# Performance work log

Measured on AMD Instinct MI355X. Metric: run time of the kernel, lower is better.

## Reference

```python
import jax, jax.numpy as jnp
import numpy as np

N = 50000      # nodes
E = 800000     # edges (avg degree 16)
F_IN = 128
# (d_in, d_out) for the 9 GCNConv layers with width=256, n_layers=3
DIMS = [(128, 128), (128, 192), (192, 256), (256, 256), (256, 256), (256, 256), (256, 192), (192, 128), (128, 1)]
# ReLU after every conv except loop conv i==n_layers-2 (conv idx 4) and the final conv
RELU = [True, True, True, True, False, True, True, True, False]


def setup_inputs() -> dict:
    key = jax.random.key(0)
    ks = jax.random.split(key, 2 + 2 * len(DIMS))
    inp = {
        "x": jax.random.normal(ks[0], (N, F_IN), dtype=jnp.float32),
        "edge_index": jax.random.randint(ks[1], (2, E), 0, N, dtype=jnp.int64),
    }
    for i, (din, dout) in enumerate(DIMS):
        # Glorot-ish init for weights, small random bias (GCNConv has bias=True)
        inp[f"W{i}"] = jax.random.normal(ks[2 + 2 * i], (din, dout), dtype=jnp.float32) / np.float32(np.sqrt(din))
        inp[f"b{i}"] = jax.random.normal(ks[3 + 2 * i], (dout,), dtype=jnp.float32) * 0.01
    return inp


def _gcn_stack(x, src_f, dst_f, norm, Ws, bs):
    h = x
    for i in range(len(Ws)):
        h = h @ Ws[i]                                  # [N, dout] dense transform first (dout <= din mostly)
        msg = h[src_f] * norm[:, None]                 # gather + edge-normalize  [E+N, dout]
        h = jax.ops.segment_sum(msg, dst_f, num_segments=N) + bs[i]
        if RELU[i]:
            h = jax.nn.relu(h)
        # Dropout layers are identity in eval/inference mode.
    return h


def reference(x, edge_index,
              W0, b0, W1, b1, W2, b2, W3, b3, W4, b4, W5, b5, W6, b6, W7, b7, W8, b8):
    src, dst = edge_index[0], edge_index[1]
    loop = jnp.arange(N, dtype=src.dtype)
    # GCNConv default: add self loops, symmetric normalization D^{-1/2}(A+I)D^{-1/2}
    src_f = jnp.concatenate([src, loop])
    dst_f = jnp.concatenate([dst, loop])
    deg = jax.ops.segment_sum(jnp.ones(E + N, dtype=x.dtype), dst_f, num_segments=N)
    dinv = jax.lax.rsqrt(jnp.maximum(deg, 1.0))        # deg >= 1 thanks to self loops
    norm = dinv[src_f] * dinv[dst_f]                   # per-edge coefficient [E+N]
    Ws = [W0, W1, W2, W3, W4, W5, W6, W7, W8]
    bs = [b0, b1, b2, b3, b4, b5, b6, b7, b8]
    return _gcn_stack(x, src_f, dst_f, norm, Ws, bs)   # [N, 1]
```

## Files before the change

kernel.cpp:

```cpp
#include <hip/hip_runtime.h>


#define TPB 256

using bf16x8 = __attribute__((ext_vector_type(8))) __bf16;
using f32x4  = __attribute__((ext_vector_type(4))) float;
using f32x2  = __attribute__((ext_vector_type(2))) float;

__device__ __forceinline__ unsigned bf16rne(float x) {
    unsigned u = __float_as_uint(x);
    return (u + 0x7fffu + ((u >> 16) & 1u)) >> 16;
}

__device__ __forceinline__ f32x2 bl2(unsigned u) {
    return (f32x2){__uint_as_float(u << 16), __uint_as_float(u & 0xffff0000u)};
}

__device__ __forceinline__ void stage16(const unsigned short* g, unsigned short* l) {
#if __has_builtin(__builtin_amdgcn_global_load_lds)
    __builtin_amdgcn_global_load_lds((const __attribute__((address_space(1))) void*)g,
                                     (__attribute__((address_space(3))) void*)l, 16, 0, 0);
#else
    *(uint4*)((char*)l + (threadIdx.x & 63) * 16) = *(const uint4*)g;
#endif
}


__global__ void zinit_kernel(int* cnt, int n) {
    int i = blockIdx.x * blockDim.x + threadIdx.x;
    if (i < n) cnt[i] = 0;
}

__global__ void count_kernel(const int* __restrict__ dst, int* __restrict__ cnt,
                             int* __restrict__ rank, int E) {
    int e = blockIdx.x * blockDim.x + threadIdx.x;
    if (e < E) rank[e] = atomicAdd(&cnt[dst[e]], 1);
}


__global__ void blockhist_kernel(const int* __restrict__ cnt, int* __restrict__ localRank,
                                 int* __restrict__ hb, float* __restrict__ dinv,
                                 int n, int nb) {
    __shared__ int h[64];
    int t = threadIdx.x;
    if (t < 64) h[t] = 0;
    __syncthreads();
    int i = blockIdx.x * TPB + t;
    if (i < n) {
        int c = cnt[i];
        dinv[i] = rsqrtf((float)(c + 1));
        int d = c; if (d > 63) d = 63;
        localRank[i] = atomicAdd(&h[d], 1);
    }
    __syncthreads();
    if (t < 64) hb[t * nb + blockIdx.x] = h[t];
}

__global__ __launch_bounds__(256) void sortscan_kernel(int* __restrict__ hb, int nb) {
    __shared__ int sh[64 * 256];
    __shared__ int tot[64], base[64];
    int t = threadIdx.x;
    int total = 64 * nb;
    for (int i = t; i < total; i += 256) sh[i] = hb[i];
    __syncthreads();
    if (t < 64) {
        int run = 0;
        for (int b = 0; b < nb; b++) {
            int v = sh[t * nb + b];
            sh[t * nb + b] = run;
            run += v;
        }
        tot[t] = run;
    }
    __syncthreads();
    if (t == 0) {
        int acc = 0;
        for (int b = 0; b < 64; b++) { base[b] = acc; acc += tot[b]; }
    }
    __syncthreads();
    for (int i = t; i < total; i += 256) hb[i] = sh[i] + base[i / nb];
}

__global__ void scatter2_kernel(const int* __restrict__ cnt,
                                const int* __restrict__ localRank, const int* __restrict__ hb,
                                int* __restrict__ perm, int* __restrict__ pcnt,
                                int* __restrict__ iperm, int n, int nb) {
    int i = blockIdx.x * TPB + threadIdx.x;
    if (i >= n) return;
    int c = cnt[i];
    int d = c; if (d > 63) d = 63;
    int pos = hb[d * nb + blockIdx.x] + localRank[i];
    perm[pos] = i;
    pcnt[pos] = c;
    iperm[i] = pos;
}

__global__ void scan1_kernel(const int* __restrict__ pcnt, int* __restrict__ prowp2,
                             int* __restrict__ bsums, int n) {
    __shared__ int sh[TPB];
    int t = threadIdx.x;
    int i = blockIdx.x * TPB + t;
    int v = (i < n) ? (pcnt[i] + 1) : 0;
    sh[t] = v;
    __syncthreads();
    for (int off = 1; off < TPB; off <<= 1) {
        int x = (t >= off) ? sh[t - off] : 0;
        __syncthreads();
        sh[t] += x;
        __syncthreads();
    }
    if (i < n) prowp2[i] = sh[t] - v;
    if (t == TPB - 1) bsums[blockIdx.x] = sh[t];
}

__global__ void scan3_kernel(int* __restrict__ rowp, const int* __restrict__ bsums,
                             int n, int nb) {
    __shared__ int sh[TPB];
    int t = threadIdx.x;
    int v = (t < nb && t < (int)blockIdx.x) ? bsums[t] : 0;
    sh[t] = v;
    __syncthreads();
    for (int off = 1; off < TPB; off <<= 1) {
        int x = (t >= off) ? sh[t - off] : 0;
        __syncthreads();
        sh[t] += x;
        __syncthreads();
    }
    int offset = sh[TPB - 1];
    int i = blockIdx.x * TPB + t;
    if (i < n) rowp[i] += offset;
}

__global__ void rowo_kernel(const int* __restrict__ iperm, const int* __restrict__ prowp2,
                            int* __restrict__ rowo, int n) {
    int i = blockIdx.x * TPB + threadIdx.x;
    if (i < n) rowo[i] = prowp2[iperm[i]];
}

__global__ void fillself_kernel(const int* __restrict__ src, const int* __restrict__ dst,
                                const int* __restrict__ rank,
                                const float* __restrict__ dinv,
                                const int* __restrict__ rowo,
                                const int* __restrict__ cnt,
                                unsigned* __restrict__ edges2, int E, int n) {
    int id = blockIdx.x * blockDim.x + threadIdx.x;
    if (id < E) {
        int s = src[id], d = dst[id];
        int pos = rowo[d] + rank[id];
        edges2[pos] = (unsigned)s | (bf16rne(dinv[s] * dinv[d]) << 16);
    } else if (id < E + n) {
        int i = id - E;
        float dv = dinv[i];
        edges2[rowo[i] + cnt[i]] = (unsigned)i | (bf16rne(dv * dv) << 16);
    }
}


struct WPtrs { const float* p[8]; };

__global__ void wtcvt_kernel(WPtrs wp, unsigned short* __restrict__ Wts,
                             const float* __restrict__ xin,
                             unsigned short* __restrict__ Bx, int n4) {
    const int cum[9] = {0, 16384, 40960, 90112, 155648, 221184, 286720, 335872, 360448};
    const int Ns[8] = {128, 192, 256, 256, 256, 256, 192, 128};
    const int Ks[8] = {128, 128, 192, 256, 256, 256, 256, 192};
    int id = blockIdx.x * blockDim.x + threadIdx.x;
    if (id < 360448) {
        int L = 0;
#pragma unroll
        for (int t = 1; t < 8; t++) if (id >= cum[t]) L = t;
        int lid = id - cum[L];
        int N = Ns[L], K = Ks[L];
        int k = lid / N, n = lid - k * N;
        Wts[cum[L] + n * K + k] = (unsigned short)bf16rne(wp.p[L][lid]);
    } else {
        int i = id - 360448;
        if (i >= n4) return;
        float4 v = ((const float4*)xin)[i];
        uint2 o;
        o.x = bf16rne(v.x) | (bf16rne(v.y) << 16);
        o.y = bf16rne(v.z) | (bf16rne(v.w) << 16);
        ((uint2*)Bx)[i] = o;
    }
}


__global__ __launch_bounds__(256) void gemm_mfma_kernel(
    const unsigned short* __restrict__ A, const unsigned short* __restrict__ Wt,
    const float* __restrict__ bias, unsigned short* __restrict__ C,
    int M, int K, int Nc, int doBias, int doRelu, int outChunked) {
    __shared__ unsigned short Qb[128 * 64];
    __shared__ unsigned short Pb[128 * 64];
    int tid = threadIdx.x;
    int l = tid & 63, w = tid >> 6;
    int node0 = blockIdx.x * 128, feat0 = blockIdx.y * 128;

    f32x4 acc[4][4];
#pragma unroll
    for (int i = 0; i < 4; i++)
#pragma unroll
        for (int j = 0; j < 4; j++) acc[i][j] = (f32x4){0.f, 0.f, 0.f, 0.f};

    const unsigned short* gQ[4];
    const unsigned short* gP[4];
    unsigned short* lQ[4];
    unsigned short* lP[4];
#pragma unroll
    for (int h = 0; h < 4; h++) {
        int slot = tid + h * 256;
        int r = slot >> 3, q = slot & 7;
        int qg = q ^ (r & 7);
        int nd = node0 + r; if (nd > M - 1) nd = M - 1;
        int ft = feat0 + r; if (ft > Nc - 1) ft = Nc - 1;
        gQ[h] = A + (size_t)nd * K + qg * 8;
        gP[h] = Wt + (size_t)ft * K + qg * 8;
        lQ[h] = Qb + (size_t)(w * 64 + h * 256) * 8;
        lP[h] = Pb + (size_t)(w * 64 + h * 256) * 8;
    }

    int q4 = l >> 4, m16 = l & 15;
    int featHalf = w & 1, nodeHalf = w >> 1;
    int rP0 = featHalf * 64 + m16;
    int rQ0 = nodeHalf * 64 + m16;
    int sw = m16 & 7;

    for (int k0 = 0; k0 < K; k0 += 64) {
        __syncthreads();
#pragma unroll
        for (int h = 0; h < 4; h++) {
            stage16(gQ[h] + k0, lQ[h]);
            stage16(gP[h] + k0, lP[h]);
        }
        __syncthreads();
#pragma unroll
        for (int ko = 0; ko < 2; ko++) {
            bf16x8 pf[4], qf[4];
#pragma unroll
            for (int i = 0; i < 4; i++)
                pf[i] = *(const bf16x8*)(Pb + (rP0 + i * 16) * 64 + ((ko * 4 + q4) ^ sw) * 8);
#pragma unroll
            for (int j = 0; j < 4; j++)
                qf[j] = *(const bf16x8*)(Qb + (rQ0 + j * 16) * 64 + ((ko * 4 + q4) ^ sw) * 8);
#pragma unroll
            for (int i = 0; i < 4; i++)
#pragma unroll
                for (int j = 0; j < 4; j++)
                    acc[i][j] = __builtin_amdgcn_mfma_f32_16x16x32_bf16(pf[i], qf[j],
                                                                        acc[i][j], 0, 0, 0);
        }
    }

#pragma unroll
    for (int i = 0; i < 4; i++) {
        int gf0 = feat0 + featHalf * 64 + i * 16 + q4 * 4;
        if (gf0 >= Nc) continue;
        float4 bv = make_float4(0.f, 0.f, 0.f, 0.f);
        if (doBias) bv = *(const float4*)(bias + gf0);
        size_t cb = outChunked ? ((size_t)(gf0 >> 6) * ((size_t)M * 64) + (gf0 & 63))
                               : (size_t)gf0;
#pragma unroll
        for (int j = 0; j < 4; j++) {
            int gn = node0 + nodeHalf * 64 + j * 16 + m16;
            if (gn >= M) continue;
            f32x4 v = acc[i][j];
            float x0 = v[0] + bv.x, x1 = v[1] + bv.y;
            float x2 = v[2] + bv.z, x3 = v[3] + bv.w;
            if (doRelu) {
                x0 = fmaxf(x0, 0.f); x1 = fmaxf(x1, 0.f);
                x2 = fmaxf(x2, 0.f); x3 = fmaxf(x3, 0.f);
            }
            uint2 o;
            o.x = bf16rne(x0) | (bf16rne(x1) << 16);
            o.y = bf16rne(x2) | (bf16rne(x3) << 16);
            size_t off = outChunked ? (cb + (size_t)gn * 64) : (cb + (size_t)gn * Nc);
            *(uint2*)(C + off) = o;
        }
    }
}

__global__ void gemv128_bf16_kernel(const unsigned short* __restrict__ A,
                                    const float* __restrict__ w,
                                    float* __restrict__ out, int M) {
    int wid = (blockIdx.x * blockDim.x + threadIdx.x) >> 6;
    int lane = threadIdx.x & 63;
    if (wid >= M) return;
    const unsigned short* a = A + (size_t)wid * 128;
    float a0 = __uint_as_float((unsigned)a[lane] << 16);
    float a1 = __uint_as_float((unsigned)a[lane + 64] << 16);
    float s = a0 * w[lane] + a1 * w[lane + 64];
#pragma unroll
    for (int off = 32; off > 0; off >>= 1) s += __shfl_down(s, off);
    if (lane == 0) out[wid] = s;
}


__global__ __launch_bounds__(256) void agg_group_kernel(
    const uint4* __restrict__ in, const int* __restrict__ prowp2,
    const int* __restrict__ pcnt, const int* __restrict__ perm,
    const unsigned* __restrict__ edges2,
    const float* __restrict__ bias, uint4* __restrict__ out,
    int Q, int upx, int ngPerUnit, int NG, int n_nodes, int rowVec4,
    int doBias, int doRelu, int outChunked) {
    int xcd = blockIdx.x & 7;
    int slot = blockIdx.x >> 3;
    int u = slot / ngPerUnit;
    int ngIdx = slot - u * ngPerUnit;
    int unit = xcd * upx + u;
    int chunk = unit / Q;
    int q = unit - chunk * Q;
    int ng = ngIdx * Q + q;
    if (ng >= NG) return;
    ng = NG - 1 - ng;

    int wave = threadIdx.x >> 6;
    int lane = threadIdx.x & 63;
    int group = lane >> 3, fl = lane & 7;
    int gb = lane & ~7;
    int i = ng * 32 + wave * 8 + group;
    if (i >= n_nodes) return;

    const uint4* sf = in + (size_t)chunk * n_nodes * 8 + fl;
    int s0 = prowp2[i];
    int c = pcnt[i] + 1;
    int node = perm[i];
    const unsigned* ep = edges2 + s0;

    f32x2 acc[2][4];
#pragma unroll
    for (int k = 0; k < 2; k++)
#pragma unroll
        for (int m = 0; m < 4; m++) acc[k][m] = (f32x2){0.f, 0.f};

    unsigned ew = (fl < c) ? ep[fl] : 0u;
    unsigned eA[4]; uint4 pA[4];
#pragma unroll
    for (int j = 0; j < 4; j++) eA[j] = (unsigned)__shfl((int)ew, gb + j);
#pragma unroll
    for (int j = 0; j < 4; j++) pA[j] = sf[(size_t)(eA[j] & 0xffffu) * 8];

    for (int base = 0; base < c; base += 8) {
        unsigned ewn = (base + 8 + fl < c) ? ep[base + 8 + fl] : 0u;
        unsigned eB[4]; uint4 pB[4];
#pragma unroll
        for (int j = 0; j < 4; j++) eB[j] = (unsigned)__shfl((int)ew, gb + 4 + j);
#pragma unroll
        for (int j = 0; j < 4; j++) pB[j] = sf[(size_t)(eB[j] & 0xffffu) * 8];
#pragma unroll
        for (int j = 0; j < 4; j++) {
            float wgt = __uint_as_float(eA[j] & 0xffff0000u);
            f32x2 w2 = {wgt, wgt};
            int k = j & 1;
            acc[k][0] += w2 * bl2(pA[j].x);
            acc[k][1] += w2 * bl2(pA[j].y);
            acc[k][2] += w2 * bl2(pA[j].z);
            acc[k][3] += w2 * bl2(pA[j].w);
        }
#pragma unroll
        for (int j = 0; j < 4; j++) eA[j] = (unsigned)__shfl((int)ewn, gb + j);
#pragma unroll
        for (int j = 0; j < 4; j++) pA[j] = sf[(size_t)(eA[j] & 0xffffu) * 8];
#pragma unroll
        for (int j = 0; j < 4; j++) {
            float wgt = __uint_as_float(eB[j] & 0xffff0000u);
            f32x2 w2 = {wgt, wgt};
            int k = j & 1;
            acc[k][0] += w2 * bl2(pB[j].x);
            acc[k][1] += w2 * bl2(pB[j].y);
            acc[k][2] += w2 * bl2(pB[j].z);
            acc[k][3] += w2 * bl2(pB[j].w);
        }
        ew = ewn;
    }
    f32x2 s[4];
#pragma unroll
    for (int m = 0; m < 4; m++) s[m] = acc[0][m] + acc[1][m];

    if (doBias) {
        const float* bp = bias + chunk * 64 + fl * 8;
        float4 b0 = *(const float4*)bp;
        float4 b1 = *(const float4*)(bp + 4);
        s[0] += (f32x2){b0.x, b0.y};
        s[1] += (f32x2){b0.z, b0.w};
        s[2] += (f32x2){b1.x, b1.y};
        s[3] += (f32x2){b1.z, b1.w};
    }
    if (doRelu) {
#pragma unroll
        for (int m = 0; m < 4; m++) {
            s[m][0] = fmaxf(s[m][0], 0.f);
            s[m][1] = fmaxf(s[m][1], 0.f);
        }
    }
    uint4 o;
    o.x = bf16rne(s[0][0]) | (bf16rne(s[0][1]) << 16);
    o.y = bf16rne(s[1][0]) | (bf16rne(s[1][1]) << 16);
    o.z = bf16rne(s[2][0]) | (bf16rne(s[2][1]) << 16);
    o.w = bf16rne(s[3][0]) | (bf16rne(s[3][1]) << 16);
    size_t oi = outChunked ? ((size_t)chunk * n_nodes * 8 + (size_t)node * 8 + fl)
                           : ((size_t)node * rowVec4 + chunk * 8 + fl);
    out[oi] = o;
}

__global__ void agg1_kernel(const float* __restrict__ in, const int* __restrict__ prowp2,
                            const int* __restrict__ pcnt, const int* __restrict__ perm,
                            const unsigned* __restrict__ edges2,
                            const float* __restrict__ bias, float* __restrict__ out,
                            int n_nodes) {
    int n = blockIdx.x * blockDim.x + threadIdx.x;
    if (n >= n_nodes) return;
    float acc = 0.f;
    int s0 = prowp2[n];
    int c = pcnt[n] + 1;
    for (int j = 0; j < c; j++) {
        unsigned e = edges2[s0 + j];
        acc += __uint_as_float(e & 0xffff0000u) * in[e & 0xffffu];
    }
    acc += bias[0];
    out[perm[n]] = acc;
}


extern "C" void kernel_launch(void* const* d_in, const int* in_sizes, int n_in,
                              void* d_out, int out_size, void* d_ws, size_t ws_size,
                              hipStream_t stream) {
    const float* x = (const float*)d_in[0];
    const int* ei = (const int*)d_in[1];
    const int Nn = in_sizes[0] / 128;
    const int E = in_sizes[1] / 2;
    const int* src = ei;
    const int* dst = ei + E;

    char* ws = (char*)d_ws;
    size_t off = 0;
    auto alloc = [&](size_t bytes) -> char* {
        char* p = ws + off;
        off = (off + bytes + 255) & ~(size_t)255;
        return p;
    };
    int* cnt = (int*)alloc((size_t)Nn * 4);
    int* rank = (int*)alloc((size_t)E * 4);
    int* bsums = (int*)alloc(1024);
    float* dinv = (float*)alloc((size_t)Nn * 4);
    int* localRank = (int*)alloc((size_t)Nn * 4);
    int* hb = (int*)alloc((size_t)64 * 256 * 4);
    int* perm = (int*)alloc((size_t)Nn * 4);
    int* pcnt = (int*)alloc((size_t)Nn * 4);
    int* iperm = (int*)alloc((size_t)Nn * 4);
    int* prowp2 = (int*)alloc((size_t)Nn * 4);
    int* rowo = (int*)alloc((size_t)Nn * 4);
    unsigned* edges2 = (unsigned*)alloc((size_t)(E + Nn + 64) * 4);
    unsigned short* T = (unsigned short*)alloc((size_t)Nn * 256 * 2);
    unsigned short* H = (unsigned short*)alloc((size_t)Nn * 256 * 2);
    unsigned short* Bx = (unsigned short*)alloc((size_t)Nn * 128 * 2);
    float* F = (float*)alloc((size_t)Nn * 4);
    unsigned short* Wts = (unsigned short*)alloc((size_t)400000 * 2);
    (void)ws_size;

    const int dims[9][2] = {{128,128},{128,192},{192,256},{256,256},{256,256},
                            {256,256},{256,192},{192,128},{128,1}};
    unsigned short* Wt[8];
    {
        size_t o = 0;
        for (int i = 0; i < 8; i++) { Wt[i] = Wts + o; o += (size_t)dims[i][0] * dims[i][1]; }
    }

    int nbN = (Nn + TPB - 1) / TPB;
    int nbE = (E + TPB - 1) / TPB;
    int nbEN = (E + Nn + TPB - 1) / TPB;

    zinit_kernel<<<nbN, TPB, 0, stream>>>(cnt, Nn);
    count_kernel<<<nbE, TPB, 0, stream>>>(dst, cnt, rank, E);
    blockhist_kernel<<<nbN, TPB, 0, stream>>>(cnt, localRank, hb, dinv, Nn, nbN);
    sortscan_kernel<<<1, 256, 0, stream>>>(hb, nbN);
    scatter2_kernel<<<nbN, TPB, 0, stream>>>(cnt, localRank, hb, perm, pcnt, iperm,
                                             Nn, nbN);
    scan1_kernel<<<nbN, TPB, 0, stream>>>(pcnt, prowp2, bsums, Nn);
    scan3_kernel<<<nbN, TPB, 0, stream>>>(prowp2, bsums, Nn, nbN);
    rowo_kernel<<<nbN, TPB, 0, stream>>>(iperm, prowp2, rowo, Nn);
    fillself_kernel<<<nbEN, TPB, 0, stream>>>(src, dst, rank, dinv, rowo, cnt,
                                              edges2, E, Nn);

    WPtrs wp;
    for (int i = 0; i < 8; i++) wp.p[i] = (const float*)d_in[2 + 2 * i];
    int n4 = Nn * 32;
    wtcvt_kernel<<<(360448 + n4 + TPB - 1) / TPB, TPB, 0, stream>>>(wp, Wts, x, Bx, n4);

    auto gemm = [&](const unsigned short* A, int i, unsigned short* C, int K, int Nc,
                    int doBias, int doRelu, int outChunked) {
        const float* b = (const float*)d_in[3 + 2 * i];
        dim3 grid((Nn + 127) / 128, (Nc + 127) / 128);
        gemm_mfma_kernel<<<grid, 256, 0, stream>>>(A, Wt[i], b, C, Nn, K, Nc,
                                                   doBias, doRelu, outChunked);
    };
    int NG = (Nn + 31) / 32;
    auto agg = [&](const unsigned short* inb, unsigned short* outb, int w, int i,
                   int doBias, int doRelu, int outChunked) {
        int nch = w / 64;
        int Q = (nch == 4) ? 2 : (nch == 3) ? 8 : 4;
        int upx = nch * Q / 8;
        int ngPerUnit = (NG + Q - 1) / Q;
        int blocksPerXcd = upx * ngPerUnit;
        const float* b = (const float*)d_in[3 + 2 * i];
        agg_group_kernel<<<blocksPerXcd * 8, 256, 0, stream>>>(
            (const uint4*)inb, prowp2, pcnt, perm, edges2, b, (uint4*)outb,
            Q, upx, ngPerUnit, NG, Nn, w / 8, doBias, doRelu, outChunked);
    };

    gemm(Bx, 0, T, 128, 128, 0, 0, 1);
    agg(T, H, 128, 0, 1, 1, 1);
    agg(H, T, 128, 1, 0, 0, 0);
    gemm(T, 1, H, 128, 192, 1, 1, 1);
    agg(H, T, 192, 2, 0, 0, 0);
    gemm(T, 2, H, 192, 256, 1, 1, 0);
    gemm(H, 3, T, 256, 256, 0, 0, 1);
    agg(T, H, 256, 3, 1, 1, 0);
    gemm(H, 4, T, 256, 256, 0, 0, 1);
    agg(T, H, 256, 4, 1, 0, 0);
    gemm(H, 5, T, 256, 256, 0, 0, 1);
    agg(T, H, 256, 5, 1, 1, 0);
    gemm(H, 6, T, 256, 192, 0, 0, 1);
    agg(T, H, 192, 6, 1, 1, 0);
    gemm(H, 7, T, 192, 128, 0, 0, 1);
    agg(T, H, 128, 7, 1, 1, 0);
    gemv128_bf16_kernel<<<(Nn + 3) / 4, 256, 0, stream>>>(H, (const float*)d_in[2 + 16],
                                                          F, Nn);
    agg1_kernel<<<nbN, TPB, 0, stream>>>(F, prowp2, pcnt, perm, edges2,
                                         (const float*)d_in[3 + 16], (float*)d_out, Nn);
}
```

Measured before the change: 578.6 us.

## Double-buffer GEMM LDS staging and swizzle block order for two feature tiles

The MFMA GEMM now double-buffers its LDS tiles, issuing the next K-slice's global-to-LDS loads before computing on the current slice, with one barrier per iteration instead of two. This is meant to hide global load latency behind MFMA work. For GEMMs with two 128-wide feature tiles, blocks are also remapped through a 1D grid so that consecutive blocks share node tiles, which should improve L2 reuse of the A rows. LDS use doubles to 64KB per block, which may reduce occupancy. The loop's only barrier now sits after the compute, and it is not clear the async global_load_lds writes are waited on before that barrier.

```diff
diff --git a/kernel.cpp b/kernel.cpp
--- a/kernel.cpp
+++ b/kernel.cpp
@@ -188,12 +188,21 @@
 __global__ __launch_bounds__(256) void gemm_mfma_kernel(
     const unsigned short* __restrict__ A, const unsigned short* __restrict__ Wt,
     const float* __restrict__ bias, unsigned short* __restrict__ C,
-    int M, int K, int Nc, int doBias, int doRelu, int outChunked) {
-    __shared__ unsigned short Qb[128 * 64];
-    __shared__ unsigned short Pb[128 * 64];
+    int M, int K, int Nc, int doBias, int doRelu, int outChunked,
+    int nTilesX, int swz) {
+    __shared__ unsigned short Qb[2][128 * 64];
+    __shared__ unsigned short Pb[2][128 * 64];
+    int bx, by;
+    if (swz) {
+        int g = blockIdx.x >> 4, r = blockIdx.x & 15;
+        bx = g * 8 + (r & 7); by = r >> 3;
+        if (bx >= nTilesX) return;
+    } else {
+        bx = blockIdx.x; by = 0;
+    }
     int tid = threadIdx.x;
     int l = tid & 63, w = tid >> 6;
-    int node0 = blockIdx.x * 128, feat0 = blockIdx.y * 128;
+    int node0 = bx * 128, feat0 = by * 128;
 
     f32x4 acc[4][4];
 #pragma unroll
@@ -203,8 +212,7 @@
 
     const unsigned short* gQ[4];
     const unsigned short* gP[4];
-    unsigned short* lQ[4];
-    unsigned short* lP[4];
+    int loff[4];
 #pragma unroll
     for (int h = 0; h < 4; h++) {
         int slot = tid + h * 256;
@@ -214,8 +222,7 @@
         int ft = feat0 + r; if (ft > Nc - 1) ft = Nc - 1;
         gQ[h] = A + (size_t)nd * K + qg * 8;
         gP[h] = Wt + (size_t)ft * K + qg * 8;
-        lQ[h] = Qb + (size_t)(w * 64 + h * 256) * 8;
-        lP[h] = Pb + (size_t)(w * 64 + h * 256) * 8;
+        loff[h] = (w * 64 + h * 256) * 8;
     }
 
     int q4 = l >> 4, m16 = l & 15;
@@ -223,24 +230,34 @@
     int rP0 = featHalf * 64 + m16;
     int rQ0 = nodeHalf * 64 + m16;
     int sw = m16 & 7;
-
-    for (int k0 = 0; k0 < K; k0 += 64) {
-        __syncthreads();
-#pragma unroll
-        for (int h = 0; h < 4; h++) {
-            stage16(gQ[h] + k0, lQ[h]);
-            stage16(gP[h] + k0, lP[h]);
-        }
-        __syncthreads();
+    int nk = K >> 6;
+
+#pragma unroll
+    for (int h = 0; h < 4; h++) {
+        stage16(gQ[h], Qb[0] + loff[h]);
+        stage16(gP[h], Pb[0] + loff[h]);
+    }
+    __syncthreads();
+
+    int cur = 0;
+    for (int t = 0; t < nk; t++) {
+        if (t + 1 < nk) {
+            int k0 = (t + 1) << 6;
+#pragma unroll
+            for (int h = 0; h < 4; h++) {
+                stage16(gQ[h] + k0, Qb[cur ^ 1] + loff[h]);
+                stage16(gP[h] + k0, Pb[cur ^ 1] + loff[h]);
+            }
+        }
 #pragma unroll
         for (int ko = 0; ko < 2; ko++) {
             bf16x8 pf[4], qf[4];
 #pragma unroll
             for (int i = 0; i < 4; i++)
-                pf[i] = *(const bf16x8*)(Pb + (rP0 + i * 16) * 64 + ((ko * 4 + q4) ^ sw) * 8);
+                pf[i] = *(const bf16x8*)(Pb[cur] + (rP0 + i * 16) * 64 + ((ko * 4 + q4) ^ sw) * 8);
 #pragma unroll
             for (int j = 0; j < 4; j++)
-                qf[j] = *(const bf16x8*)(Qb + (rQ0 + j * 16) * 64 + ((ko * 4 + q4) ^ sw) * 8);
+                qf[j] = *(const bf16x8*)(Qb[cur] + (rQ0 + j * 16) * 64 + ((ko * 4 + q4) ^ sw) * 8);
 #pragma unroll
             for (int i = 0; i < 4; i++)
 #pragma unroll
@@ -248,6 +265,8 @@
                     acc[i][j] = __builtin_amdgcn_mfma_f32_16x16x32_bf16(pf[i], qf[j],
                                                                         acc[i][j], 0, 0, 0);
         }
+        __syncthreads();
+        cur ^= 1;
     }
 
 #pragma unroll
@@ -485,12 +504,21 @@
     int n4 = Nn * 32;
     wtcvt_kernel<<<(360448 + n4 + TPB - 1) / TPB, TPB, 0, stream>>>(wp, Wts, x, Bx, n4);
 
+    int ntx = (Nn + 127) / 128;
     auto gemm = [&](const unsigned short* A, int i, unsigned short* C, int K, int Nc,
                     int doBias, int doRelu, int outChunked) {
         const float* b = (const float*)d_in[3 + 2 * i];
-        dim3 grid((Nn + 127) / 128, (Nc + 127) / 128);
-        gemm_mfma_kernel<<<grid, 256, 0, stream>>>(A, Wt[i], b, C, Nn, K, Nc,
-                                                   doBias, doRelu, outChunked);
+        int nyt = (Nc + 127) / 128;
+        if (nyt == 2) {
+            int ng = (ntx + 7) / 8;
+            gemm_mfma_kernel<<<ng * 16, 256, 0, stream>>>(A, Wt[i], b, C, Nn, K, Nc,
+                                                          doBias, doRelu, outChunked,
+                                                          ntx, 1);
+        } else {
+            gemm_mfma_kernel<<<ntx, 256, 0, stream>>>(A, Wt[i], b, C, Nn, K, Nc,
+                                                      doBias, doRelu, outChunked,
+                                                      ntx, 0);
+        }
     };
     int NG = (Nn + 31) / 32;
     auto agg = [&](const unsigned short* inb, unsigned short* outb, int w, int i,
```

Result: no change. 575.6 us (-0.5%).

## Rewrite GEMM as full-width tiles with double-buffered LDS staging

Applied to the files above, without the earlier changes.

Replaces the 128x128-tiled MFMA GEMM with a templated kernel in which each 512-thread block computes all output features (128/192/256) for 128 nodes. The K loop now steps by 32 and uses a double-buffered LDS ping-pong, so the next K slice is staged while MFMAs run on the current one, with one barrier per step. This removes the second grid dimension, so activation rows are loaded once instead of once per feature tile. The cost is more accumulator registers per thread (launch bounds 512,4) and less parallelism per tile.

```diff
diff --git a/kernel.cpp b/kernel.cpp
--- a/kernel.cpp
+++ b/kernel.cpp
@@ -185,75 +185,79 @@
 }
 
 
-__global__ __launch_bounds__(256) void gemm_mfma_kernel(
+template<int NFR>
+__global__ __launch_bounds__(512, 4) void gemm2_kernel(
     const unsigned short* __restrict__ A, const unsigned short* __restrict__ Wt,
     const float* __restrict__ bias, unsigned short* __restrict__ C,
-    int M, int K, int Nc, int doBias, int doRelu, int outChunked) {
-    __shared__ unsigned short Qb[128 * 64];
-    __shared__ unsigned short Pb[128 * 64];
+    int M, int K, int doBias, int doRelu, int outChunked) {
+    constexpr int Nc = NFR * 64;
+    __shared__ unsigned short Qb[2][128 * 32];
+    __shared__ unsigned short Pb[2][Nc * 32];
     int tid = threadIdx.x;
     int l = tid & 63, w = tid >> 6;
-    int node0 = blockIdx.x * 128, feat0 = blockIdx.y * 128;
-
-    f32x4 acc[4][4];
-#pragma unroll
-    for (int i = 0; i < 4; i++)
-#pragma unroll
-        for (int j = 0; j < 4; j++) acc[i][j] = (f32x4){0.f, 0.f, 0.f, 0.f};
-
-    const unsigned short* gQ[4];
-    const unsigned short* gP[4];
-    unsigned short* lQ[4];
-    unsigned short* lP[4];
-#pragma unroll
-    for (int h = 0; h < 4; h++) {
-        int slot = tid + h * 256;
-        int r = slot >> 3, q = slot & 7;
-        int qg = q ^ (r & 7);
-        int nd = node0 + r; if (nd > M - 1) nd = M - 1;
-        int ft = feat0 + r; if (ft > Nc - 1) ft = Nc - 1;
-        gQ[h] = A + (size_t)nd * K + qg * 8;
-        gP[h] = Wt + (size_t)ft * K + qg * 8;
-        lQ[h] = Qb + (size_t)(w * 64 + h * 256) * 8;
-        lP[h] = Pb + (size_t)(w * 64 + h * 256) * 8;
-    }
+    int node0 = blockIdx.x * 128;
+
+    f32x4 acc[4][NFR];
+#pragma unroll
+    for (int j = 0; j < 4; j++)
+#pragma unroll
+        for (int f = 0; f < NFR; f++) acc[j][f] = (f32x4){0.f, 0.f, 0.f, 0.f};
+
+    int rA = tid >> 2, qA = tid & 3;
+    int nd = node0 + rA; if (nd > M - 1) nd = M - 1;
+    const unsigned short* gA = A + (size_t)nd * K + (qA ^ (rA & 3)) * 8;
+    const unsigned short* gW0 = Wt + (size_t)rA * K + (qA ^ (rA & 3)) * 8;
+    const unsigned short* gW1 = gW0;
+    if (NFR >= 3) {
+        int rW1 = 128 + rA;
+        gW1 = Wt + (size_t)rW1 * K + (qA ^ (rW1 & 3)) * 8;
+    }
+    int lB = w * 512;
 
     int q4 = l >> 4, m16 = l & 15;
-    int featHalf = w & 1, nodeHalf = w >> 1;
-    int rP0 = featHalf * 64 + m16;
+    int nodeHalf = w >> 2, fq = w & 3;
     int rQ0 = nodeHalf * 64 + m16;
-    int sw = m16 & 7;
-
-    for (int k0 = 0; k0 < K; k0 += 64) {
+    int rP0 = fq * (NFR * 16) + m16;
+    int swq8 = (q4 ^ (m16 & 3)) * 8;
+    int nk = K >> 5;
+
+    {
+        stage16(gA, Qb[0] + lB);
+        stage16(gW0, Pb[0] + lB);
+        if constexpr (NFR == 4) stage16(gW1, Pb[0] + 4096 + lB);
+        else if constexpr (NFR == 3) { if (w < 4) stage16(gW1, Pb[0] + 4096 + lB); }
+    }
+    __syncthreads();
+
+    int cur = 0;
+    for (int t = 0; t < nk; t++) {
+        if (t + 1 < nk) {
+            int k0 = (t + 1) << 5;
+            stage16(gA + k0, Qb[cur ^ 1] + lB);
+            stage16(gW0 + k0, Pb[cur ^ 1] + lB);
+            if constexpr (NFR == 4) stage16(gW1 + k0, Pb[cur ^ 1] + 4096 + lB);
+            else if constexpr (NFR == 3) { if (w < 4) stage16(gW1 + k0, Pb[cur ^ 1] + 4096 + lB); }
+        }
+        bf16x8 qf[4], pf[NFR];
+#pragma unroll
+        for (int j = 0; j < 4; j++)
+            qf[j] = *(const bf16x8*)(Qb[cur] + (rQ0 + j * 16) * 32 + swq8);
+#pragma unroll
+        for (int f = 0; f < NFR; f++)
+            pf[f] = *(const bf16x8*)(Pb[cur] + (rP0 + f * 16) * 32 + swq8);
+#pragma unroll
+        for (int j = 0; j < 4; j++)
+#pragma unroll
+            for (int f = 0; f < NFR; f++)
+                acc[j][f] = __builtin_amdgcn_mfma_f32_16x16x32_bf16(pf[f], qf[j],
+                                                                    acc[j][f], 0, 0, 0);
         __syncthreads();
-#pragma unroll
-        for (int h = 0; h < 4; h++) {
-            stage16(gQ[h] + k0, lQ[h]);
-            stage16(gP[h] + k0, lP[h]);
-        }
-        __syncthreads();
-#pragma unroll
-        for (int ko = 0; ko < 2; ko++) {
-            bf16x8 pf[4], qf[4];
-#pragma unroll
-            for (int i = 0; i < 4; i++)
-                pf[i] = *(const bf16x8*)(Pb + (rP0 + i * 16) * 64 + ((ko * 4 + q4) ^ sw) * 8);
-#pragma unroll
-            for (int j = 0; j < 4; j++)
-                qf[j] = *(const bf16x8*)(Qb + (rQ0 + j * 16) * 64 + ((ko * 4 + q4) ^ sw) * 8);
-#pragma unroll
-            for (int i = 0; i < 4; i++)
-#pragma unroll
-                for (int j = 0; j < 4; j++)
-                    acc[i][j] = __builtin_amdgcn_mfma_f32_16x16x32_bf16(pf[i], qf[j],
-                                                                        acc[i][j], 0, 0, 0);
-        }
-    }
-
-#pragma unroll
-    for (int i = 0; i < 4; i++) {
-        int gf0 = feat0 + featHalf * 64 + i * 16 + q4 * 4;
-        if (gf0 >= Nc) continue;
+        cur ^= 1;
+    }
+
+#pragma unroll
+    for (int f = 0; f < NFR; f++) {
+        int gf0 = fq * (NFR * 16) + f * 16 + q4 * 4;
         float4 bv = make_float4(0.f, 0.f, 0.f, 0.f);
         if (doBias) bv = *(const float4*)(bias + gf0);
         size_t cb = outChunked ? ((size_t)(gf0 >> 6) * ((size_t)M * 64) + (gf0 & 63))
@@ -262,7 +266,7 @@
         for (int j = 0; j < 4; j++) {
             int gn = node0 + nodeHalf * 64 + j * 16 + m16;
             if (gn >= M) continue;
-            f32x4 v = acc[i][j];
+            f32x4 v = acc[j][f];
             float x0 = v[0] + bv.x, x1 = v[1] + bv.y;
             float x2 = v[2] + bv.z, x3 = v[3] + bv.w;
             if (doRelu) {
@@ -485,12 +489,19 @@
     int n4 = Nn * 32;
     wtcvt_kernel<<<(360448 + n4 + TPB - 1) / TPB, TPB, 0, stream>>>(wp, Wts, x, Bx, n4);
 
+    int ntx = (Nn + 127) / 128;
     auto gemm = [&](const unsigned short* A, int i, unsigned short* C, int K, int Nc,
                     int doBias, int doRelu, int outChunked) {
         const float* b = (const float*)d_in[3 + 2 * i];
-        dim3 grid((Nn + 127) / 128, (Nc + 127) / 128);
-        gemm_mfma_kernel<<<grid, 256, 0, stream>>>(A, Wt[i], b, C, Nn, K, Nc,
-                                                   doBias, doRelu, outChunked);
+        if (Nc == 256)
+            gemm2_kernel<4><<<ntx, 512, 0, stream>>>(A, Wt[i], b, C, Nn, K,
+                                                     doBias, doRelu, outChunked);
+        else if (Nc == 192)
+            gemm2_kernel<3><<<ntx, 512, 0, stream>>>(A, Wt[i], b, C, Nn, K,
+                                                     doBias, doRelu, outChunked);
+        else
+            gemm2_kernel<2><<<ntx, 512, 0, stream>>>(A, Wt[i], b, C, Nn, K,
+                                                     doBias, doRelu, outChunked);
     };
     int NG = (Nn + 31) / 32;
     auto agg = [&](const unsigned short* inb, unsigned short* outb, int w, int i,
```

After: 559.3 us (median of 2 runs). 3.3% less time.
